# Kernel tuning notes

Measured on AMD Instinct MI355X. Metric: run time of the kernel, lower is better.

## Reference

```python
import jax, jax.numpy as jnp
import numpy as np

T, DM = 2048, 2048
H, KV, D = 16, 2, 128
E, I_MOE, I_SH = 16, 768, 768
TOP_K, N_GROUP, TOPK_GROUP = 4, 4, 2
ROPE_THETA = 1e6
EPS = 1e-5
ROUTED_SCALE = 1.0


def rmsnorm(x, w):
    v = jnp.mean(x * x, axis=-1, keepdims=True)
    return x * jax.lax.rsqrt(v + EPS) * w


def apply_rope(x, pos):
    # partial rotary: first D//2 dims rotated (neox style), rest passthrough
    rd = D // 2
    half = rd // 2
    inv = 1.0 / (ROPE_THETA ** (jnp.arange(0, rd, 2, dtype=jnp.float32) / rd))
    freqs = pos.astype(jnp.float32)[:, None] * inv  # [T, half]
    cos = jnp.cos(freqs)[:, None, :]
    sin = jnp.sin(freqs)[:, None, :]
    x1, x2 = x[..., :half], x[..., half:rd]
    rot = jnp.concatenate([x1 * cos - x2 * sin, x2 * cos + x1 * sin], axis=-1)
    return jnp.concatenate([rot, x[..., rd:]], axis=-1)


def mlp(x, wgu, wd):
    g, u = jnp.split(x @ wgu, 2, axis=-1)
    return (jax.nn.silu(g) * u) @ wd


def attention(x, pos, w_qkv, b_qkv, w_o, q_norm_w, k_norm_w):
    qkv = x @ w_qkv + b_qkv
    q, k, v = jnp.split(qkv, [H * D, H * D + KV * D], axis=-1)
    q = rmsnorm(q.reshape(T, H, D), q_norm_w)
    k = rmsnorm(k.reshape(T, KV, D), k_norm_w)
    v = v.reshape(T, KV, D)
    q = apply_rope(q, pos)
    k = apply_rope(k, pos)
    rep = H // KV
    k = jnp.repeat(k, rep, axis=1)
    v = jnp.repeat(v, rep, axis=1)
    scores = jnp.einsum('thd,shd->hts', q, k) * (D ** -0.5)
    causal = pos[:, None] >= pos[None, :]
    scores = jnp.where(causal[None], scores, jnp.finfo(scores.dtype).min)
    p = jax.nn.softmax(scores, axis=-1)
    o = jnp.einsum('hts,shd->thd', p, v).reshape(T, H * D)
    return o @ w_o


def moe(x, gate_w, gate_bias, shared_wgu, shared_wd, expert_wgu, expert_wd):
    # sigmoid grouped top-k routing with e_score_correction_bias (DeepSeek/GLM style)
    logits = x.astype(jnp.float32) @ gate_w
    scores = jax.nn.sigmoid(logits)
    sb = scores + gate_bias
    g = sb.reshape(T, N_GROUP, E // N_GROUP)
    group_scores = jnp.sum(jax.lax.top_k(g, 2)[0], axis=-1)  # [T, n_group]
    _, gi = jax.lax.top_k(group_scores, TOPK_GROUP)
    gmask = jnp.zeros((T, N_GROUP)).at[jnp.arange(T)[:, None], gi].set(1.0)
    emask = jnp.repeat(gmask, E // N_GROUP, axis=1)
    masked = jnp.where(emask > 0, sb, -jnp.inf)
    _, idx = jax.lax.top_k(masked, TOP_K)  # [T, top_k]
    w = jnp.take_along_axis(scores, idx, axis=1)
    w = w / jnp.sum(w, axis=1, keepdims=True)  # renormalize (norm_topk_prob)
    cw = jnp.zeros((T, E)).at[jnp.arange(T)[:, None], idx].add(w)  # dense combine weights
    gu = jnp.einsum('td,edi->tei', x, expert_wgu)  # [T, E, 2I]
    gt, ut = jnp.split(gu, 2, axis=-1)
    act = jax.nn.silu(gt) * ut * cw[:, :, None]
    routed = jnp.einsum('tei,eid->td', act, expert_wd)
    shared = mlp(x, shared_wgu, shared_wd)
    return routed * ROUTED_SCALE + shared


def setup_inputs() -> dict:
    key = jax.random.key(0)
    ks = jax.random.split(key, 12)
    s = 0.02
    return {
        'positions': jnp.arange(T, dtype=jnp.int32),
        'hidden_states': jax.random.normal(ks[0], (T, DM), jnp.float32),
        'residual': jax.random.normal(ks[1], (T, DM), jnp.float32),
        'ln1_w': jnp.ones((DM,), jnp.float32),
        'ln2_w': jnp.ones((DM,), jnp.float32),
        'w_qkv': jax.random.normal(ks[2], (DM, (H + 2 * KV) * D), jnp.float32) * s,
        'b_qkv': jnp.zeros(((H + 2 * KV) * D,), jnp.float32),
        'w_o': jax.random.normal(ks[3], (H * D, DM), jnp.float32) * s,
        'q_norm_w': jnp.ones((D,), jnp.float32),
        'k_norm_w': jnp.ones((D,), jnp.float32),
        'gate_w': jax.random.normal(ks[4], (DM, E), jnp.float32) * s,
        'gate_bias': jax.random.normal(ks[5], (E,), jnp.float32) * 0.1,
        'shared_wgu': jax.random.normal(ks[6], (DM, 2 * I_SH), jnp.float32) * s,
        'shared_wd': jax.random.normal(ks[7], (I_SH, DM), jnp.float32) * s,
        'expert_wgu': jax.random.normal(ks[8], (E, DM, 2 * I_MOE), jnp.float32) * s,
        'expert_wd': jax.random.normal(ks[9], (E, I_MOE, DM), jnp.float32) * s,
    }


def reference(positions, hidden_states, residual, ln1_w, ln2_w, w_qkv, b_qkv, w_o,
              q_norm_w, k_norm_w, gate_w, gate_bias, shared_wgu, shared_wd,
              expert_wgu, expert_wd):
    # fused add + RMSNorm (residual is not None path)
    residual = hidden_states + residual
    h = rmsnorm(residual, ln1_w)
    h = attention(h, positions, w_qkv, b_qkv, w_o, q_norm_w, k_norm_w)
    residual = h + residual
    h = rmsnorm(residual, ln2_w)
    h = moe(h, gate_w, gate_bias, shared_wgu, shared_wd, expert_wgu, expert_wd)
    return h, residual
```

## Files before the change

kernel.cpp:

```cpp
#include <hip/hip_runtime.h>
#include <stdint.h>
#include <math.h>

#define T_ 2048
#define DM 2048
#define NH 16
#define NKV 2
#define HD 128
#define QKVN 2560
#define NE 16
#define IM 768
#define ISH 768
#define MAXROWS 10240
#define ROWS_ALL 12288
#define NBLK 136
#define SM_SCALE 0.08838834764831845f

typedef __attribute__((ext_vector_type(8))) short short8;
typedef __attribute__((ext_vector_type(4))) float f32x4;

__device__ __forceinline__ float bf2f(unsigned short u){ return __uint_as_float(((unsigned int)u)<<16); }
__device__ __forceinline__ unsigned short f2bf(float f){
  unsigned int u = __float_as_uint(f);
  return (unsigned short)((u + 0x7FFFu + ((u>>16)&1u)) >> 16);
}
__device__ __forceinline__ void split2(float x, unsigned short& hi, unsigned short& lo){
  hi = f2bf(x);
  lo = f2bf(x - bf2f(hi));
}

__device__ __forceinline__ void gload16(const void* g, void* l){
  __builtin_amdgcn_global_load_lds((const __attribute__((address_space(1))) unsigned int*)g,
                                   (__attribute__((address_space(3))) unsigned int*)l, 16, 0, 0);
}

__device__ __forceinline__ int xcd_swz(int bid, int nwg){
  int q = nwg >> 3, r = nwg & 7, x = bid & 7, p = bid >> 3;
  return (x < r ? x*(q+1) : r*(q+1) + (x-r)*q) + p;
}

#define BAR()    asm volatile("s_barrier" ::: "memory")
#define VW(N)    asm volatile("s_waitcnt vmcnt(" #N ")" ::: "memory")
#define LW0()    do{ asm volatile("s_waitcnt lgkmcnt(0)" ::: "memory"); __builtin_amdgcn_sched_barrier(0); }while(0)

template<bool ILV>
__global__ void k_tconv(const float* __restrict__ src, unsigned short* __restrict__ dst,
                        const float* __restrict__ srcS, unsigned short* __restrict__ dstS,
                        int R, int C, size_t sS, size_t sD){
  int z = blockIdx.z;
  if (srcS && z == gridDim.z-1){ src = srcS; dst = dstS; }
  else { src += (size_t)z * sS; dst += (size_t)z * sD; }
  __shared__ float tile[64*65];
  int tid = threadIdx.x;
  int r0 = blockIdx.y*64, c0 = blockIdx.x*64;
  int lr = tid>>4, lc = (tid&15)*4;
  #pragma unroll
  for (int j=0;j<4;j++){
    int row = j*16 + lr;
    float4 v = *(const float4*)&src[(size_t)(r0+row)*C + c0 + lc];
    float* t = &tile[row*65 + lc];
    t[0]=v.x; t[1]=v.y; t[2]=v.z; t[3]=v.w;
  }
  __syncthreads();
  #pragma unroll
  for (int jj=0;jj<2;jj++){
    int slot = jj*256 + tid;
    int c = slot>>3, ro = (slot&7)*8;
    int cg = c0 + c;
    int cd = cg;
    if (ILV){ int b = cg>>3, inner = cg&7; cd = (b<96 ? b*16 : (b-96)*16+8) + inner; }
    short8 o;
    #pragma unroll
    for (int k=0;k<8;k++) o[k] = (short)f2bf(tile[(ro+k)*65 + c]);
    *(short8*)&dst[(size_t)cd*R + r0 + ro] = o;
  }
}

__global__ void k_tconv2(const float* __restrict__ srcA, unsigned short* __restrict__ dhiA,
                         unsigned short* __restrict__ dloA,
                         const float* __restrict__ srcB, unsigned short* __restrict__ dhiB,
                         unsigned short* __restrict__ dloB){
  const float* src; unsigned short* dhi; unsigned short* dlo; int R, C;
  if (blockIdx.z == 0){ src = srcA; dhi = dhiA; dlo = dloA; R = DM; C = QKVN; }
  else {
    if (blockIdx.x >= DM/64) return;
    src = srcB; dhi = dhiB; dlo = dloB; R = DM; C = DM;
  }
  __shared__ float tile[64*65];
  int tid = threadIdx.x;
  int r0 = blockIdx.y*64, c0 = blockIdx.x*64;
  int lr = tid>>4, lc = (tid&15)*4;
  #pragma unroll
  for (int j=0;j<4;j++){
    int row = j*16 + lr;
    float4 v = *(const float4*)&src[(size_t)(r0+row)*C + c0 + lc];
    float* t = &tile[row*65 + lc];
    t[0]=v.x; t[1]=v.y; t[2]=v.z; t[3]=v.w;
  }
  __syncthreads();
  #pragma unroll
  for (int jj=0;jj<2;jj++){
    int slot = jj*256 + tid;
    int c = slot>>3, ro = (slot&7)*8;
    short8 oh, ol;
    #pragma unroll
    for (int k=0;k<8;k++){
      unsigned short h_, l_;
      split2(tile[(ro+k)*65 + c], h_, l_);
      oh[k] = (short)h_; ol[k] = (short)l_;
    }
    size_t o = (size_t)(c0+c)*R + r0 + ro;
    *(short8*)&dhi[o] = oh;
    *(short8*)&dlo[o] = ol;
  }
}

template<bool ROUTE>
__global__ void k_add_rmsnorm(const float* __restrict__ a, const float* __restrict__ b,
                              const float* __restrict__ w, float* __restrict__ resout,
                              unsigned short* __restrict__ ohi, unsigned short* __restrict__ olo,
                              unsigned short* __restrict__ obf,
                              const float* __restrict__ gw, const float* __restrict__ gbias,
                              int* __restrict__ idx4, float* __restrict__ w4){
  int t = blockIdx.x, tid = threadIdx.x;
  const float4* a4 = (const float4*)(a + (size_t)t*DM);
  const float4* b4 = (const float4*)(b + (size_t)t*DM);
  float4 va = a4[tid], vb = b4[tid];
  float4 wa = a4[tid+256], wb = b4[tid+256];
  float4 v0, v1;
  v0.x=va.x+vb.x; v0.y=va.y+vb.y; v0.z=va.z+vb.z; v0.w=va.w+vb.w;
  v1.x=wa.x+wb.x; v1.y=wa.y+wb.y; v1.z=wa.z+wb.z; v1.w=wa.w+wb.w;
  float s = v0.x*v0.x+v0.y*v0.y+v0.z*v0.z+v0.w*v0.w
          + v1.x*v1.x+v1.y*v1.y+v1.z*v1.z+v1.w*v1.w;
  #pragma unroll
  for (int o=32;o;o>>=1) s += __shfl_xor(s,o);
  __shared__ float sm[4];
  if ((tid&63)==0) sm[tid>>6]=s;
  __syncthreads();
  s = sm[0]+sm[1]+sm[2]+sm[3];
  float rs = rsqrtf(s*(1.f/(float)DM) + 1e-5f);
  ((float4*)(resout + (size_t)t*DM))[tid] = v0;
  ((float4*)(resout + (size_t)t*DM))[tid+256] = v1;
  const float4* w4p_ = (const float4*)w;
  float4 w0 = w4p_[tid], w1 = w4p_[tid+256];
  float n[8] = { v0.x*rs*w0.x, v0.y*rs*w0.y, v0.z*rs*w0.z, v0.w*rs*w0.w,
                 v1.x*rs*w1.x, v1.y*rs*w1.y, v1.z*rs*w1.z, v1.w*rs*w1.w };
  if (ohi){
    ushort4 h0,h1,l0,l1;
    split2(n[0],h0.x,l0.x); split2(n[1],h0.y,l0.y); split2(n[2],h0.z,l0.z); split2(n[3],h0.w,l0.w);
    split2(n[4],h1.x,l1.x); split2(n[5],h1.y,l1.y); split2(n[6],h1.z,l1.z); split2(n[7],h1.w,l1.w);
    ((ushort4*)(ohi + (size_t)t*DM))[tid] = h0;
    ((ushort4*)(ohi + (size_t)t*DM))[tid+256] = h1;
    ((ushort4*)(olo + (size_t)t*DM))[tid] = l0;
    ((ushort4*)(olo + (size_t)t*DM))[tid+256] = l1;
  }
  if (obf){
    ushort4 o0 = make_ushort4(f2bf(n[0]),f2bf(n[1]),f2bf(n[2]),f2bf(n[3]));
    ushort4 o1 = make_ushort4(f2bf(n[4]),f2bf(n[5]),f2bf(n[6]),f2bf(n[7]));
    ((ushort4*)(obf + (size_t)t*DM))[tid] = o0;
    ((ushort4*)(obf + (size_t)t*DM))[tid+256] = o1;
  }
  if constexpr (ROUTE){
    __shared__ float xrow[DM];
    __shared__ float red[16][17];
    #pragma unroll
    for (int jj=0;jj<4;jj++) xrow[4*tid+jj] = n[jj];
    #pragma unroll
    for (int jj=0;jj<4;jj++) xrow[1024+4*tid+jj] = n[4+jj];
    __syncthreads();
    int e = tid & 15, grp = tid >> 4;
    float part = 0.f;
    #pragma unroll 8
    for (int c = grp; c < DM; c += 16)
      part += xrow[c] * gw[(size_t)c*16 + e];
    red[grp][e] = part;
    __syncthreads();
    if (tid==0){
      float sc[16], sb[16];
      for (int ee=0;ee<16;ee++){
        float lg = 0.f;
        for (int g2=0;g2<16;g2++) lg += red[g2][ee];
        sc[ee] = 1.f/(1.f+expf(-lg));
        sb[ee] = sc[ee] + gbias[ee];
      }
      float gs[4];
      for (int g=0;g<4;g++){
        float m1=-3.4e38f, m2=-3.4e38f;
        for (int j=0;j<4;j++){
          float v = sb[g*4+j];
          if (v>m1){ m2=m1; m1=v; } else if (v>m2) m2=v;
        }
        gs[g]=m1+m2;
      }
      int g1=0; for (int g=1;g<4;g++) if (gs[g]>gs[g1]) g1=g;
      int g2=-1; for (int g=0;g<4;g++){ if (g==g1) continue; if (g2<0 || gs[g]>gs[g2]) g2=g; }
      float msk[16];
      for (int ee=0;ee<16;ee++){ int g=ee>>2; msk[ee] = (g==g1||g==g2)? sb[ee] : -3.4e38f; }
      int id[4]; float wv[4]; float wsum=0.f;
      for (int s2=0;s2<4;s2++){
        int bb=0; float bv=-3.5e38f;
        for (int ee=0;ee<16;ee++) if (msk[ee]>bv){ bv=msk[ee]; bb=ee; }
        id[s2]=bb; wv[s2]=sc[bb]; wsum+=sc[bb]; msk[bb]=-3.5e38f;
      }
      float invs = 1.f/wsum;
      for (int s2=0;s2<4;s2++){
        idx4[t*4+s2]=id[s2];
        w4[t*4+s2]=wv[s2]*invs;
      }
    }
  }
}

template<bool GATHER, bool ACT>
__global__ __launch_bounds__(256) void k_gemm2(
    const unsigned short* __restrict__ A, const unsigned short* __restrict__ Be,
    const unsigned short* __restrict__ Bsh, unsigned short* __restrict__ C,
    int K, int lda, int ldb, int ldc,
    const int* __restrict__ offs, size_t sBe, const int* __restrict__ tok){
  int nx = gridDim.x;
  int nwg = nx * gridDim.y;
  int wid_ = xcd_swz(blockIdx.x + nx*blockIdx.y, nwg);
  int tN = wid_ % nx, tM = wid_ / nx;
  int rb = tM*128;
  if (rb >= offs[17]) return;
  const unsigned short* B;
  if (rb >= offs[16]) B = Bsh;
  else {
    int e=0;
    for (; e<15; ++e) if (offs[e+1] > rb) break;
    B = Be + (size_t)e*sBe;
  }
  __shared__ __align__(16) unsigned short As[2][4096];
  __shared__ __align__(16) unsigned short Bs[2][4096];
  int tid = threadIdx.x, lane = tid & 63, wwid = tid >> 6;
  int wr = wwid >> 1, wc = wwid & 1;
  const unsigned short* Bb = B + (size_t)tN*128*ldb;

  const unsigned short* Asrc0;
  const unsigned short* Asrc1;
  int r0s = tid>>2, r1s = r0s + 64;
  {
    if (GATHER){
      Asrc0 = A + (size_t)tok[rb + r0s]*lda;
      Asrc1 = A + (size_t)tok[rb + r1s]*lda;
    } else {
      Asrc0 = A + (size_t)(rb + r0s)*lda;
      Asrc1 = A + (size_t)(rb + r1s)*lda;
    }
  }
  int kc = tid&3;
  int sw = (r0s>>1)&3;
  int kcS = (kc ^ sw)*8;

  f32x4 acc[4][4];
  #pragma unroll
  for (int m=0;m<4;m++)
    #pragma unroll
    for (int n=0;n<4;n++) acc[m][n] = (f32x4){0.f,0.f,0.f,0.f};

  auto STAGE = [&](int b, int k0){
    gload16(Asrc0 + k0 + kcS, As[b] + (size_t)tid*8);
    gload16(Asrc1 + k0 + kcS, As[b] + (size_t)(256+tid)*8);
    gload16(Bb + (size_t)r0s*ldb + k0 + kcS, Bs[b] + (size_t)tid*8);
    gload16(Bb + (size_t)r1s*ldb + k0 + kcS, Bs[b] + (size_t)(256+tid)*8);
  };

  int nt = K >> 5, L = nt - 1;
  STAGE(0, 0);
  if (L >= 1) STAGE(1, 32);
  int i15 = lane & 15, g = lane >> 4;
  for (int i=0; i<nt; ++i){
    int cur = i & 1;
    if (i < L) { VW(4); } else { VW(0); }
    BAR();
    short8 af[4], bfr[4];
    #pragma unroll
    for (int m=0;m<4;m++){
      int row = wr*64 + m*16 + i15;
      int geff = g ^ ((row>>1)&3);
      af[m] = *(const short8*)(As[cur] + row*32 + geff*8);
    }
    #pragma unroll
    for (int n=0;n<4;n++){
      int row = wc*64 + n*16 + i15;
      int geff = g ^ ((row>>1)&3);
      bfr[n] = *(const short8*)(Bs[cur] + row*32 + geff*8);
    }
    LW0();
    BAR();
    if (i + 2 <= L) STAGE(cur, (i+2)*32);
    __builtin_amdgcn_s_setprio(1);
    #pragma unroll
    for (int m=0;m<4;m++)
      #pragma unroll
      for (int n=0;n<4;n++)
        acc[m][n] = __builtin_amdgcn_mfma_f32_16x16x32_bf16(af[m], bfr[n], acc[m][n], 0,0,0);
    __builtin_amdgcn_s_setprio(0);
  }

  if (ACT){
    int rbase = rb + wr*64, cb = tN*128 + wc*64;
    #pragma unroll
    for (int m=0;m<4;m++){
      int r0 = rbase + m*16 + ((lane>>4)<<2);
      #pragma unroll
      for (int n=0;n<4;n++){
        int f = ((cb + n*16)>>1) + (lane&7);
        #pragma unroll
        for (int r=0;r<4;r++){
          float v = acc[m][n][r];
          float vp = __shfl_xor(v, 8);
          if (!(lane&8)){
            float gg = v;
            float a = gg/(1.f+__expf(-gg))*vp;
            C[(size_t)(r0+r)*ldc + f] = f2bf(a);
          }
        }
      }
    }
  } else {
    int rbase = rb + wr*64, cb = tN*128 + wc*64;
    #pragma unroll
    for (int m=0;m<4;m++){
      int r0 = rbase + m*16 + ((lane>>4)<<2);
      #pragma unroll
      for (int n=0;n<4;n++){
        int c = cb + n*16 + (lane&15);
        #pragma unroll
        for (int r=0;r<4;r++) C[(size_t)(r0+r)*ldc + c] = f2bf(acc[m][n][r]);
      }
    }
  }
}

__global__ __launch_bounds__(256) void k_gemm_hp(
    const unsigned short* __restrict__ Ah, const unsigned short* __restrict__ Al,
    const unsigned short* __restrict__ Bh, const unsigned short* __restrict__ Bl,
    float* __restrict__ Cf,
    int K, int lda, int ldb, int ldc){
  int nx = gridDim.x, nwg = nx*gridDim.y;
  int w = xcd_swz(blockIdx.x + nx*blockIdx.y, nwg);
  int tN = w % nx, tM = w / nx;

  __shared__ __align__(16) unsigned short AsH[2][4096], AsL[2][4096];
  __shared__ __align__(16) unsigned short BsH[2][4096], BsL[2][4096];
  int tid = threadIdx.x, lane = tid & 63, wid = tid >> 6;
  int wr = wid >> 1, wc = wid & 1;
  const unsigned short* Abh = Ah + (size_t)tM*128*lda;
  const unsigned short* Abl = Al + (size_t)tM*128*lda;
  const unsigned short* Bbh = Bh + (size_t)tN*128*ldb;
  const unsigned short* Bbl = Bl + (size_t)tN*128*ldb;

  f32x4 acc[4][4];
  #pragma unroll
  for (int m=0;m<4;m++)
    #pragma unroll
    for (int n=0;n<4;n++) acc[m][n] = (f32x4){0.f,0.f,0.f,0.f};

  auto STAGE = [&](int b, int k0){
    #pragma unroll
    for (int j=0;j<2;j++){
      int cb = j*256 + tid;
      int row = cb>>2, kc = cb&3;
      int kcS = (kc ^ ((row>>1)&3))*8;
      size_t go = (size_t)row*lda + k0 + kcS;
      gload16(Abh + go, AsH[b] + (size_t)cb*8);
      gload16(Abl + go, AsL[b] + (size_t)cb*8);
      size_t bo = (size_t)row*ldb + k0 + kcS;
      gload16(Bbh + bo, BsH[b] + (size_t)cb*8);
      gload16(Bbl + bo, BsL[b] + (size_t)cb*8);
    }
  };

  int nt = K >> 5, L = nt - 1;
  STAGE(0, 0);
  if (L >= 1) STAGE(1, 32);
  int i15 = lane & 15, g = lane >> 4;
  for (int i=0; i<nt; ++i){
    int cur = i & 1;
    if (i < L) { VW(8); } else { VW(0); }
    BAR();
    short8 afh[4], afl[4], bfh[4], bfl[4];
    #pragma unroll
    for (int m=0;m<4;m++){
      int row = wr*64 + m*16 + i15;
      int ro = row*32 + (g ^ ((row>>1)&3))*8;
      afh[m] = *(const short8*)(AsH[cur] + ro);
      afl[m] = *(const short8*)(AsL[cur] + ro);
    }
    #pragma unroll
    for (int n=0;n<4;n++){
      int row = wc*64 + n*16 + i15;
      int ro = row*32 + (g ^ ((row>>1)&3))*8;
      bfh[n] = *(const short8*)(BsH[cur] + ro);
      bfl[n] = *(const short8*)(BsL[cur] + ro);
    }
    LW0();
    BAR();
    if (i + 2 <= L) STAGE(cur, (i+2)*32);
    __builtin_amdgcn_s_setprio(1);
    #pragma unroll
    for (int m=0;m<4;m++)
      #pragma unroll
      for (int n=0;n<4;n++){
        acc[m][n] = __builtin_amdgcn_mfma_f32_16x16x32_bf16(afh[m], bfh[n], acc[m][n], 0,0,0);
        acc[m][n] = __builtin_amdgcn_mfma_f32_16x16x32_bf16(afh[m], bfl[n], acc[m][n], 0,0,0);
        acc[m][n] = __builtin_amdgcn_mfma_f32_16x16x32_bf16(afl[m], bfh[n], acc[m][n], 0,0,0);
      }
    __builtin_amdgcn_s_setprio(0);
  }

  int rb = tM*128 + wr*64, cb = tN*128 + wc*64;
  #pragma unroll
  for (int m=0;m<4;m++){
    int r0 = rb + m*16 + ((lane>>4)<<2);
    #pragma unroll
    for (int n=0;n<4;n++){
      int c = cb + n*16 + (lane&15);
      #pragma unroll
      for (int r=0;r<4;r++) Cf[(size_t)(r0+r)*ldc + c] = acc[m][n][r];
    }
  }
}

__global__ __launch_bounds__(256) void k_qk_pers(
    const unsigned short* __restrict__ Qh, const unsigned short* __restrict__ Ql,
    const unsigned short* __restrict__ Kh, const unsigned short* __restrict__ Kl,
    float* __restrict__ Sp){
  int bb = blockIdx.x;
  int t0, ntile;
  if (bb < 128){ t0 = bb*9; ntile = 9; }
  else { t0 = 1152 + (bb-128)*8; ntile = 8; }
  const int ldq = NH*HD, ldk = NKV*HD;

  __shared__ __align__(16) unsigned short QsH[16384], QsL[16384];
  __shared__ __align__(16) unsigned short BsH[2][4096], BsL[2][4096];

  int tid = threadIdx.x, lane = tid & 63, wid = tid >> 6;
  int wr = wid >> 1, wc = wid & 1;
  int i15 = lane & 15, g = lane >> 4;

  f32x4 acc[4][4];
  #pragma unroll
  for (int m=0;m<4;m++)
    #pragma unroll
    for (int n=0;n<4;n++) acc[m][n] = (f32x4){0.f,0.f,0.f,0.f};

  int curZ = -1, curM = -1;
  const unsigned short* Kbh = Kh;
  const unsigned short* Kbl = Kl;
  int ti = 0;
  while (ti < ntile){
    int f = t0 + ti;
    int z = f / 136;
    int idx = f - z*136;
    int tM = 0;
    while ((tM+1)*(tM+2)/2 <= idx) tM++;
    int tri = tM*(tM+1)/2;
    int tnS = idx - tri;
    int run = ntile - ti;
    { int rem = tM+1 - tnS; if (rem < run) run = rem; }

    if (z != curZ || tM != curM){
      BAR();
      const unsigned short* Qbh = Qh + (size_t)(tM*128)*ldq + (size_t)z*HD;
      const unsigned short* Qbl = Ql + (size_t)(tM*128)*ldq + (size_t)z*HD;
      #pragma unroll
      for (int j=0;j<8;j++){
        int gi = j*256 + tid;
        int chunk = gi >> 9;
        int row = (gi >> 2) & 127;
        int gg = gi & 3;
        int col = chunk*32 + (gg ^ ((row>>1)&3))*8;
        gload16(Qbh + (size_t)row*ldq + col, QsH + (size_t)gi*8);
        gload16(Qbl + (size_t)row*ldq + col, QsL + (size_t)gi*8);
      }
      curZ = z; curM = tM;
      Kbh = Kh + (size_t)(z>>3)*HD;
      Kbl = Kl + (size_t)(z>>3)*HD;
    }

    auto BSTAGE = [&](int b, int ci){
      int tn = tnS + (ci >> 2), c = ci & 3;
      const unsigned short* sh = Kbh + (size_t)(tn*128)*ldk;
      const unsigned short* sl = Kbl + (size_t)(tn*128)*ldk;
      #pragma unroll
      for (int j=0;j<2;j++){
        int gi = j*256 + tid;
        int row = gi >> 2, gg = gi & 3;
        int col = c*32 + (gg ^ ((row>>1)&3))*8;
        gload16(sh + (size_t)row*ldk + col, BsH[b] + (size_t)gi*8);
        gload16(sl + (size_t)row*ldk + col, BsL[b] + (size_t)gi*8);
      }
    };

    int NC = run*4;
    BSTAGE(0, 0);
    BSTAGE(1, 1);
    for (int ci=0; ci<NC; ++ci){
      int cur = ci & 1, c = ci & 3, tn = tnS + (ci >> 2);
      if (ci < NC-1) { VW(4); } else { VW(0); }
      BAR();
      short8 afh[4], afl[4], bfh[4], bfl[4];
      #pragma unroll
      for (int m=0;m<4;m++){
        int row = wr*64 + m*16 + i15;
        int ro = c*4096 + row*32 + (g ^ ((row>>1)&3))*8;
        afh[m] = *(const short8*)(QsH + ro);
        afl[m] = *(const short8*)(QsL + ro);
      }
      #pragma unroll
      for (int n=0;n<4;n++){
        int row = wc*64 + n*16 + i15;
        int ro = row*32 + (g ^ ((row>>1)&3))*8;
        bfh[n] = *(const short8*)(BsH[cur] + ro);
        bfl[n] = *(const short8*)(BsL[cur] + ro);
      }
      LW0();
      BAR();
      if (ci + 2 < NC) BSTAGE(cur, ci+2);
      __builtin_amdgcn_s_setprio(1);
      #pragma unroll
      for (int m=0;m<4;m++)
        #pragma unroll
        for (int n=0;n<4;n++){
          acc[m][n] = __builtin_amdgcn_mfma_f32_16x16x32_bf16(afh[m], bfh[n], acc[m][n], 0,0,0);
          acc[m][n] = __builtin_amdgcn_mfma_f32_16x16x32_bf16(afh[m], bfl[n], acc[m][n], 0,0,0);
          acc[m][n] = __builtin_amdgcn_mfma_f32_16x16x32_bf16(afl[m], bfh[n], acc[m][n], 0,0,0);
        }
      __builtin_amdgcn_s_setprio(0);
      if (c == 3){
        float* Cb = Sp + ((size_t)z*NBLK + tri + tn)*16384;
        #pragma unroll
        for (int m=0;m<4;m++){
          int r0 = wr*64 + m*16 + (g<<2);
          #pragma unroll
          for (int n=0;n<4;n++){
            int ccol = wc*64 + n*16 + i15;
            #pragma unroll
            for (int r=0;r<4;r++) Cb[(size_t)(r0+r)*128 + ccol] = acc[m][n][r];
          }
        }
        #pragma unroll
        for (int m=0;m<4;m++)
          #pragma unroll
          for (int n=0;n<4;n++) acc[m][n] = (f32x4){0.f,0.f,0.f,0.f};
      }
    }
    ti += run;
  }
}

__global__ __launch_bounds__(256) void k_pv_hp(
    const float* __restrict__ Sp,
    const unsigned short* __restrict__ Vh, const unsigned short* __restrict__ Vl,
    float* __restrict__ part, float* __restrict__ rsums){
  int c = blockIdx.x, tM = blockIdx.y, z = blockIdx.z;
  int kbeg = c*512;
  int kend = min((tM+1)*128, (c+1)*512);
  if (kbeg >= kend) return;
  int tMk = tM*128;
  size_t tri = (size_t)tM*(tM+1)/2;
  const float* Ab = Sp + ((size_t)z*NBLK + tri)*16384;
  const unsigned short* Bbh = Vh + (size_t)(z>>3)*HD*T_;
  const unsigned short* Bbl = Vl + (size_t)(z>>3)*HD*T_;

  __shared__ __align__(16) float Asf[2][4096];
  __shared__ __align__(16) unsigned short BsH[2][4096], BsL[2][4096];
  int tid = threadIdx.x, lane = tid & 63, wid = tid >> 6;
  int wr = wid >> 1, wc = wid & 1;
  int i15 = lane & 15, g2 = (lane>>4)*2;

  int r0s = tid>>2, r1s = r0s + 64;
  int kcB = ((tid&3) ^ ((r0s>>1)&3))*8;
  int rowA = tid>>3, gA = tid&7;

  f32x4 acc[4][4];
  #pragma unroll
  for (int m=0;m<4;m++)
    #pragma unroll
    for (int n=0;n<4;n++) acc[m][n] = (f32x4){0.f,0.f,0.f,0.f};
  float rsum[4] = {0.f,0.f,0.f,0.f};

  auto STAGE = [&](int b, int k0){
    #pragma unroll
    for (int j=0;j<4;j++){
      int r = j*32 + rowA;
      int gS = gA ^ (r & 7);
      size_t ga = (size_t)(k0>>7)*16384 + (size_t)r*128 + (k0&127) + gS*4;
      gload16(Ab + ga, Asf[b] + ((size_t)j*256 + tid)*4);
    }
    size_t bo0 = (size_t)r0s*T_ + k0 + kcB;
    size_t bo1 = (size_t)r1s*T_ + k0 + kcB;
    gload16(Bbh + bo0, BsH[b] + (size_t)tid*8);
    gload16(Bbh + bo1, BsH[b] + (size_t)(256+tid)*8);
    gload16(Bbl + bo0, BsL[b] + (size_t)tid*8);
    gload16(Bbl + bo1, BsL[b] + (size_t)(256+tid)*8);
  };

  int nt = (kend - kbeg) >> 5, L = nt - 1;
  STAGE(0, kbeg);
  if (L >= 1) STAGE(1, kbeg + 32);
  for (int i=0; i<nt; ++i){
    int cur = i & 1;
    int k0 = kbeg + i*32;
    if (i < L) { VW(8); } else { VW(0); }
    BAR();
    int diag = (k0 >= tMk);
    short8 afh[4], afl[4], bfh[4], bfl[4];
    #pragma unroll
    for (int m=0;m<4;m++){
      int r = wr*64 + m*16 + i15;
      int s0 = r*8 + ((g2  ) ^ (r&7));
      int s1 = r*8 + ((g2+1) ^ (r&7));
      f32x4 a0 = *(const f32x4*)(Asf[cur] + s0*4);
      f32x4 a1 = *(const f32x4*)(Asf[cur] + s1*4);
      float pv[8] = {a0[0],a0[1],a0[2],a0[3],a1[0],a1[1],a1[2],a1[3]};
      if (diag){
        int kb = k0 & 127;
        #pragma unroll
        for (int j=0;j<8;j++){
          int kl = kb + ((j<4) ? g2*4 + j : (g2+1)*4 + (j-4));
          if (kl > r) pv[j] = -3.0e38f;
        }
      }
      short8 h8, l8;
      #pragma unroll
      for (int j=0;j<8;j++){
        float p = __expf(pv[j]*SM_SCALE);
        rsum[m] += p;
        unsigned short hh, ll; split2(p, hh, ll);
        h8[j] = (short)hh; l8[j] = (short)ll;
      }
      afh[m] = h8; afl[m] = l8;
    }
    #pragma unroll
    for (int n=0;n<4;n++){
      int row = wc*64 + n*16 + i15;
      int ro = row*32 + ((lane>>4) ^ ((row>>1)&3))*8;
      bfh[n] = *(const short8*)(BsH[cur] + ro);
      bfl[n] = *(const short8*)(BsL[cur] + ro);
    }
    LW0();
    BAR();
    if (i + 2 <= L) STAGE(cur, kbeg + (i+2)*32);
    __builtin_amdgcn_s_setprio(1);
    #pragma unroll
    for (int m=0;m<4;m++)
      #pragma unroll
      for (int n=0;n<4;n++){
        acc[m][n] = __builtin_amdgcn_mfma_f32_16x16x32_bf16(afh[m], bfh[n], acc[m][n], 0,0,0);
        acc[m][n] = __builtin_amdgcn_mfma_f32_16x16x32_bf16(afh[m], bfl[n], acc[m][n], 0,0,0);
        acc[m][n] = __builtin_amdgcn_mfma_f32_16x16x32_bf16(afl[m], bfh[n], acc[m][n], 0,0,0);
      }
    __builtin_amdgcn_s_setprio(0);
  }

  #pragma unroll
  for (int m=0;m<4;m++){
    float v = rsum[m];
    v += __shfl_xor(v, 16);
    v += __shfl_xor(v, 32);
    if ((lane>>4)==0 && wc==0)
      rsums[((size_t)c*NH + z)*T_ + tMk + wr*64 + m*16 + i15] = v;
  }

  float* Cb = part + (size_t)c*T_*DM + (size_t)tMk*DM + (size_t)z*HD;
  #pragma unroll
  for (int m=0;m<4;m++){
    int r0 = wr*64 + m*16 + ((lane>>4)<<2);
    #pragma unroll
    for (int n=0;n<4;n++){
      int ccol = wc*64 + n*16 + (lane&15);
      #pragma unroll
      for (int r=0;r<4;r++) Cb[(size_t)(r0+r)*DM + ccol] = acc[m][n][r];
    }
  }
}

__global__ void k_pv_reduce(const float* __restrict__ part, const float* __restrict__ rsums,
                            unsigned short* __restrict__ aoh, unsigned short* __restrict__ aol){
  int t = blockIdx.x, tid = threadIdx.x;
  int nc = ((t>>7) + 4) >> 2;
  #pragma unroll
  for (int half=0; half<2; ++half){
    int idx = tid + half*256;
    int z = idx >> 5;
    float tot = 0.f;
    for (int c=0; c<nc; ++c) tot += rsums[((size_t)c*NH + z)*T_ + t];
    float inv = 1.f / tot;
    float4 s = ((const float4*)(part + (size_t)t*DM))[idx];
    for (int c=1; c<nc; ++c){
      float4 v = ((const float4*)(part + (size_t)c*T_*DM + (size_t)t*DM))[idx];
      s.x+=v.x; s.y+=v.y; s.z+=v.z; s.w+=v.w;
    }
    s.x*=inv; s.y*=inv; s.z*=inv; s.w*=inv;
    ushort4 h_, l_;
    split2(s.x,h_.x,l_.x); split2(s.y,h_.y,l_.y); split2(s.z,h_.z,l_.z); split2(s.w,h_.w,l_.w);
    ((ushort4*)(aoh + (size_t)t*DM))[idx] = h_;
    ((ushort4*)(aol + (size_t)t*DM))[idx] = l_;
  }
}

__global__ void k_qkv_post_hp(const float* __restrict__ qkv, const float* __restrict__ bias,
                              const float* __restrict__ qnw, const float* __restrict__ knw,
                              const int* __restrict__ pos_,
                              unsigned short* __restrict__ qhi, unsigned short* __restrict__ qlo,
                              unsigned short* __restrict__ khi, unsigned short* __restrict__ klo,
                              unsigned short* __restrict__ vThi, unsigned short* __restrict__ vTlo){
  int t = blockIdx.x;
  int half = threadIdx.x >> 7;
  int d = threadIdx.x & 127;
  int wseg = (threadIdx.x >> 6) & 1;
  float posf = (float)pos_[t];
  __shared__ float buf[2][128];
  __shared__ float ssum[2][2];
  __shared__ float inv_sh[32];
  if (threadIdx.x < 32)
    inv_sh[threadIdx.x] = (float)pow(1000000.0, -(double)threadIdx.x/32.0);
  __syncthreads();
  for (int it=0; it<10; ++it){
    int seg = it*2 + half;
    float x = qkv[(size_t)t*QKVN + seg*128 + d] + bias[seg*128 + d];
    float p = x*x;
    #pragma unroll
    for (int o=32;o;o>>=1) p += __shfl_xor(p,o);
    if ((threadIdx.x&63)==0) ssum[half][wseg] = p;
    __syncthreads();
    float rs = rsqrtf((ssum[half][0]+ssum[half][1])*(1.f/128.f) + 1e-5f);
    float w = (seg<16) ? qnw[d] : ((seg<18) ? knw[d] : 1.f);
    float nv = x*rs*w;
    buf[half][d] = nv;
    __syncthreads();
    float outv = (seg<18) ? nv : x;
    if (seg < 18 && d < 64){
      int i = d & 31;
      float ang = posf * inv_sh[i];
      float sn, cs; sincosf(ang, &sn, &cs);
      if (d < 32) outv = nv*cs - buf[half][d+32]*sn;
      else        outv = nv*cs + buf[half][d-32]*sn;
    }
    unsigned short h_, l_; split2(outv, h_, l_);
    if (seg < 16){ size_t o = ((size_t)t*NH + seg)*HD + d; qhi[o]=h_; qlo[o]=l_; }
    else if (seg < 18){ size_t o = ((size_t)t*NKV + (seg-16))*HD + d; khi[o]=h_; klo[o]=l_; }
    else { size_t o = ((size_t)(seg-18)*HD + d)*T_ + t; vThi[o]=h_; vTlo[o]=l_; }
    __syncthreads();
  }
}

__global__ void k_offplace(const int* __restrict__ idx4, int* __restrict__ offs,
                           int* __restrict__ rrow, int* __restrict__ tok){
  __shared__ int hist[16];
  __shared__ int hoff[16];
  __shared__ int fill[16];
  int tid = threadIdx.x;
  if (tid < 16) hist[tid] = 0;
  __syncthreads();
  for (int i = tid; i < ROWS_ALL; i += 256) tok[i] = 0;
  for (int i = tid; i < T_*4; i += 256)
    atomicAdd(&hist[idx4[i]], 1);
  __syncthreads();
  if (tid == 0){
    int o = 0;
    for (int e=0;e<16;e++){ hoff[e]=o; offs[e]=o; o += ((hist[e]+127)>>7)<<7; }
    offs[16]=o;
    offs[17]=o + T_;
  }
  if (tid < 16) fill[tid] = 0;
  __syncthreads();
  int off16 = offs[16];
  for (int t = tid; t < T_; t += 256){
    #pragma unroll
    for (int s=0;s<4;s++){
      int e = idx4[t*4+s];
      int p = atomicAdd(&fill[e],1);
      int r = hoff[e]+p;
      rrow[t*4+s]=r;
      tok[r]=t;
    }
    tok[off16+t] = t;
  }
}

__global__ void k_combine(const unsigned short* __restrict__ eout,
                          const int* __restrict__ rrow, const float* __restrict__ w4,
                          const int* __restrict__ offs, float* __restrict__ outh){
  int t = blockIdx.x;
  int rs = offs[16] + t;
  int r0=rrow[t*4+0], r1=rrow[t*4+1], r2=rrow[t*4+2], r3=rrow[t*4+3];
  float w0=w4[t*4+0], w1=w4[t*4+1], w2=w4[t*4+2], w3=w4[t*4+3];
  for (int d=threadIdx.x; d<DM; d+=256){
    float v = bf2f(eout[(size_t)rs*DM+d])
            + w0*bf2f(eout[(size_t)r0*DM+d]) + w1*bf2f(eout[(size_t)r1*DM+d])
            + w2*bf2f(eout[(size_t)r2*DM+d]) + w3*bf2f(eout[(size_t)r3*DM+d]);
    outh[(size_t)t*DM+d] = v;
  }
}

extern "C" void kernel_launch(void* const* d_in, const int* in_sizes, int n_in,
                              void* d_out, int out_size, void* d_ws, size_t ws_size,
                              hipStream_t stream){
  const int*   positions = (const int*)d_in[0];
  const float* hidden    = (const float*)d_in[1];
  const float* residual  = (const float*)d_in[2];
  const float* ln1       = (const float*)d_in[3];
  const float* ln2       = (const float*)d_in[4];
  const float* w_qkv     = (const float*)d_in[5];
  const float* b_qkv     = (const float*)d_in[6];
  const float* w_o       = (const float*)d_in[7];
  const float* qnw       = (const float*)d_in[8];
  const float* knw       = (const float*)d_in[9];
  const float* gate_w    = (const float*)d_in[10];
  const float* gate_b    = (const float*)d_in[11];
  const float* sh_wgu    = (const float*)d_in[12];
  const float* sh_wd     = (const float*)d_in[13];
  const float* e_wgu     = (const float*)d_in[14];
  const float* e_wd      = (const float*)d_in[15];
  float* out_h   = (float*)d_out;
  float* out_res = (float*)d_out + (size_t)T_*DM;

  char* ws = (char*)d_ws;
  size_t off = 0;
  auto alloc = [&](size_t b){ size_t r = off; off += (b + 255) & ~(size_t)255; return r; };

  size_t o_h2b  = alloc((size_t)T_*DM*2);
  size_t o_idx  = alloc((size_t)T_*4*4);
  size_t o_w4   = alloc((size_t)T_*4*4);
  size_t o_offs = alloc(72);
  size_t o_rrow = alloc((size_t)T_*4*4);
  size_t o_tok  = alloc((size_t)ROWS_ALL*4);

  size_t U0 = off;
  size_t a = U0;
  auto allocA = [&](size_t b){ size_t r = a; a += (b + 255) & ~(size_t)255; return r; };
  size_t o_h1h  = allocA((size_t)T_*DM*2);
  size_t o_h1l  = allocA((size_t)T_*DM*2);
  size_t o_wqh  = allocA((size_t)QKVN*DM*2);
  size_t o_wql  = allocA((size_t)QKVN*DM*2);
  size_t o_qkvf = allocA((size_t)T_*QKVN*4);
  size_t o_qh   = allocA((size_t)T_*NH*HD*2);
  size_t o_ql   = allocA((size_t)T_*NH*HD*2);
  size_t o_kh   = allocA((size_t)T_*NKV*HD*2);
  size_t o_kl   = allocA((size_t)T_*NKV*HD*2);
  size_t o_vth  = allocA((size_t)NKV*HD*T_*2);
  size_t o_vtl  = allocA((size_t)NKV*HD*T_*2);
  size_t o_woh  = allocA((size_t)DM*DM*2);
  size_t o_wol  = allocA((size_t)DM*DM*2);
  size_t o_aoh  = allocA((size_t)T_*DM*2);
  size_t o_aol  = allocA((size_t)T_*DM*2);
  size_t o_attnP= allocA((size_t)T_*DM*4);
  size_t o_rsum = allocA((size_t)4*NH*T_*4);
  size_t o_Sp   = allocA((size_t)NH*NBLK*16384*4);
  size_t o_pvp  = allocA((size_t)4*T_*DM*4);
  size_t b_ = U0;
  auto allocB = [&](size_t b){ size_t r = b_; b_ += (b + 255) & ~(size_t)255; return r; };
  size_t o_ewgu = allocB((size_t)NE*2*IM*DM*2);
  size_t o_ewd  = allocB((size_t)NE*DM*IM*2);
  size_t o_shgu = allocB((size_t)2*ISH*DM*2);
  size_t o_shwd = allocB((size_t)DM*ISH*2);
  size_t o_actx = allocB((size_t)ROWS_ALL*IM*2);
  size_t o_eout = allocB((size_t)ROWS_ALL*DM*2);

  unsigned short* h2b   = (unsigned short*)(ws+o_h2b);
  int*   idx4  = (int*)(ws+o_idx);
  float* w4p   = (float*)(ws+o_w4);
  int*   offs  = (int*)(ws+o_offs);
  int*   rrow  = (int*)(ws+o_rrow);
  int*   tok   = (int*)(ws+o_tok);
  unsigned short* h1h = (unsigned short*)(ws+o_h1h);
  unsigned short* h1l = (unsigned short*)(ws+o_h1l);
  unsigned short* wqh = (unsigned short*)(ws+o_wqh);
  unsigned short* wql = (unsigned short*)(ws+o_wql);
  float*          qkvf= (float*)(ws+o_qkvf);
  unsigned short* qh  = (unsigned short*)(ws+o_qh);
  unsigned short* ql  = (unsigned short*)(ws+o_ql);
  unsigned short* kh  = (unsigned short*)(ws+o_kh);
  unsigned short* kl  = (unsigned short*)(ws+o_kl);
  unsigned short* vth = (unsigned short*)(ws+o_vth);
  unsigned short* vtl = (unsigned short*)(ws+o_vtl);
  unsigned short* woh = (unsigned short*)(ws+o_woh);
  unsigned short* wol = (unsigned short*)(ws+o_wol);
  unsigned short* aoh = (unsigned short*)(ws+o_aoh);
  unsigned short* aol = (unsigned short*)(ws+o_aol);
  float*          attnP=(float*)(ws+o_attnP);
  float*          rsums=(float*)(ws+o_rsum);
  float*          Sp  = (float*)(ws+o_Sp);
  float*          pvpart = (float*)(ws+o_pvp);
  unsigned short* ewguT=(unsigned short*)(ws+o_ewgu);
  unsigned short* ewdT = (unsigned short*)(ws+o_ewd);
  unsigned short* shguT=(unsigned short*)(ws+o_shgu);
  unsigned short* shwdT=(unsigned short*)(ws+o_shwd);
  unsigned short* actx= (unsigned short*)(ws+o_actx);
  unsigned short* eout= (unsigned short*)(ws+o_eout);

  k_tconv2<<<dim3(QKVN/64, DM/64, 2),256,0,stream>>>(w_qkv, wqh, wql, w_o, woh, wol);

  k_add_rmsnorm<false><<<T_,256,0,stream>>>(hidden, residual, ln1, out_res, h1h, h1l, nullptr,
                                            nullptr, nullptr, nullptr, nullptr);

  k_gemm_hp<<<dim3(QKVN/128,T_/128,1),256,0,stream>>>(
      h1h, h1l, wqh, wql, qkvf, DM, DM, DM, QKVN);
  k_qkv_post_hp<<<T_,256,0,stream>>>(qkvf, b_qkv, qnw, knw, positions, qh, ql, kh, kl, vth, vtl);

  k_qk_pers<<<dim3(256),256,0,stream>>>(qh, ql, kh, kl, Sp);
  k_pv_hp<<<dim3(4,T_/128,NH),256,0,stream>>>(Sp, vth, vtl, pvpart, rsums);
  k_pv_reduce<<<T_,256,0,stream>>>(pvpart, rsums, aoh, aol);
  k_gemm_hp<<<dim3(DM/128,T_/128,1),256,0,stream>>>(
      aoh, aol, woh, wol, attnP, DM, DM, DM, DM);

  k_add_rmsnorm<true><<<T_,256,0,stream>>>(attnP, out_res, ln2, out_res, nullptr, nullptr, h2b,
                                           gate_w, gate_b, idx4, w4p);

  k_offplace<<<1,256,0,stream>>>(idx4, offs, rrow, tok);

  k_tconv<true ><<<dim3(2*IM/64, DM/64, NE+1),256,0,stream>>>(
      e_wgu, ewguT, sh_wgu, shguT, DM, 2*IM, (size_t)DM*2*IM, (size_t)2*IM*DM);
  k_tconv<false><<<dim3(DM/64, IM/64, NE+1),256,0,stream>>>(
      e_wd,  ewdT,  sh_wd,  shwdT, IM, DM,   (size_t)IM*DM,   (size_t)DM*IM);

  k_gemm2<true, true ><<<dim3(2*IM/128, ROWS_ALL/128, 1),256,0,stream>>>(
      h2b, ewguT, shguT, actx, DM, DM, DM, IM, offs, (size_t)2*IM*DM, tok);
  k_gemm2<false, false><<<dim3(DM/128, ROWS_ALL/128, 1),256,0,stream>>>(
      actx, ewdT, shwdT, eout, IM, IM, IM, DM, offs, (size_t)DM*IM, nullptr);

  k_combine<<<T_,256,0,stream>>>(eout, rrow, w4p, offs, out_h);
}
```

Measured before the change: 664.4 us.

## Merge weight conversions and routing offsets into one kernel; balance PV split

Folds the two MoE weight transpose/convert kernels and the single-block offset/placement kernel into one launch, with the offset work done by a spare block. This removes two launches and hides the serial one-block kernel behind the conversion work. Separately, the PV kernel now splits the causal key range evenly into 128-wide tiles across a number of chunks that depends on the row tile, instead of fixed 512-wide chunks, to balance work. The trade-off is a larger grid with idle blocks, and the offset work now runs inside one block of a busy kernel.

```diff
diff --git a/kernel.cpp b/kernel.cpp
--- a/kernel.cpp
+++ b/kernel.cpp
@@ -43,16 +43,66 @@
 #define VW(N)    asm volatile("s_waitcnt vmcnt(" #N ")" ::: "memory")
 #define LW0()    do{ asm volatile("s_waitcnt lgkmcnt(0)" ::: "memory"); __builtin_amdgcn_sched_barrier(0); }while(0)
 
-template<bool ILV>
-__global__ void k_tconv(const float* __restrict__ src, unsigned short* __restrict__ dst,
-                        const float* __restrict__ srcS, unsigned short* __restrict__ dstS,
-                        int R, int C, size_t sS, size_t sD){
-  int z = blockIdx.z;
-  if (srcS && z == gridDim.z-1){ src = srcS; dst = dstS; }
-  else { src += (size_t)z * sS; dst += (size_t)z * sD; }
+__device__ void do_offplace(const int* __restrict__ idx4, int* __restrict__ offs,
+                            int* __restrict__ rrow, int* __restrict__ tok){
+  __shared__ int hist[16];
+  __shared__ int hoff[16];
+  __shared__ int fill[16];
+  int tid = threadIdx.x;
+  if (tid < 16) hist[tid] = 0;
+  __syncthreads();
+  for (int i = tid; i < ROWS_ALL; i += 256) tok[i] = 0;
+  for (int i = tid; i < T_*4; i += 256)
+    atomicAdd(&hist[idx4[i]], 1);
+  __syncthreads();
+  if (tid == 0){
+    int o = 0;
+    for (int e=0;e<16;e++){ hoff[e]=o; offs[e]=o; o += ((hist[e]+127)>>7)<<7; }
+    offs[16]=o;
+    offs[17]=o + T_;
+  }
+  if (tid < 16) fill[tid] = 0;
+  __syncthreads();
+  int off16 = offs[16];
+  for (int t = tid; t < T_; t += 256){
+    #pragma unroll
+    for (int s=0;s<4;s++){
+      int e = idx4[t*4+s];
+      int p = atomicAdd(&fill[e],1);
+      int r = hoff[e]+p;
+      rrow[t*4+s]=r;
+      tok[r]=t;
+    }
+    tok[off16+t] = t;
+  }
+}
+
+__global__ void k_wconv(const float* __restrict__ e_wgu, unsigned short* __restrict__ ewguT,
+                        const float* __restrict__ sh_wgu, unsigned short* __restrict__ shguT,
+                        const float* __restrict__ e_wd, unsigned short* __restrict__ ewdT,
+                        const float* __restrict__ sh_wd, unsigned short* __restrict__ shwdT,
+                        const int* __restrict__ idx4, int* __restrict__ offs,
+                        int* __restrict__ rrow, int* __restrict__ tok){
   __shared__ float tile[64*65];
+  int z = blockIdx.z, x = blockIdx.x, y = blockIdx.y;
   int tid = threadIdx.x;
-  int r0 = blockIdx.y*64, c0 = blockIdx.x*64;
+  const float* src; unsigned short* dst;
+  int R, C, r0, c0;
+  bool ilv;
+  if (x < 24){
+    src = (z==16)? sh_wgu : e_wgu + (size_t)z*((size_t)DM*2*IM);
+    dst = (z==16)? shguT : ewguT + (size_t)z*((size_t)2*IM*DM);
+    R = DM; C = 2*IM; r0 = y*64; c0 = x*64; ilv = true;
+  } else {
+    int flat = (x-24) + 24*y;
+    if (flat >= 384){
+      if (z==16 && x==47 && y==31) do_offplace(idx4, offs, rrow, tok);
+      return;
+    }
+    src = (z==16)? sh_wd : e_wd + (size_t)z*((size_t)IM*DM);
+    dst = (z==16)? shwdT : ewdT + (size_t)z*((size_t)DM*IM);
+    R = IM; C = DM; r0 = (flat/32)*64; c0 = (flat%32)*64; ilv = false;
+  }
   int lr = tid>>4, lc = (tid&15)*4;
   #pragma unroll
   for (int j=0;j<4;j++){
@@ -68,7 +118,7 @@
     int c = slot>>3, ro = (slot&7)*8;
     int cg = c0 + c;
     int cd = cg;
-    if (ILV){ int b = cg>>3, inner = cg&7; cd = (b<96 ? b*16 : (b-96)*16+8) + inner; }
+    if (ilv){ int b = cg>>3, inner = cg&7; cd = (b<96 ? b*16 : (b-96)*16+8) + inner; }
     short8 o;
     #pragma unroll
     for (int k=0;k<8;k++) o[k] = (short)f2bf(tile[(ro+k)*65 + c]);
@@ -556,9 +606,14 @@
     const unsigned short* __restrict__ Vh, const unsigned short* __restrict__ Vl,
     float* __restrict__ part, float* __restrict__ rsums){
   int c = blockIdx.x, tM = blockIdx.y, z = blockIdx.z;
-  int kbeg = c*512;
-  int kend = min((tM+1)*128, (c+1)*512);
-  if (kbeg >= kend) return;
+  int nc = (tM+4)>>2;
+  if (c >= nc) return;
+  int ntile = tM+1;
+  int base = ntile/nc, rem = ntile - base*nc;
+  int start = c*base + (c<rem ? c : rem);
+  int len = base + (c<rem ? 1 : 0);
+  int kbeg = start*128;
+  int kend = kbeg + len*128;
   int tMk = tM*128;
   size_t tri = (size_t)tM*(tM+1)/2;
   const float* Ab = Sp + ((size_t)z*NBLK + tri)*16384;
@@ -745,40 +800,6 @@
     else if (seg < 18){ size_t o = ((size_t)t*NKV + (seg-16))*HD + d; khi[o]=h_; klo[o]=l_; }
     else { size_t o = ((size_t)(seg-18)*HD + d)*T_ + t; vThi[o]=h_; vTlo[o]=l_; }
     __syncthreads();
-  }
-}
-
-__global__ void k_offplace(const int* __restrict__ idx4, int* __restrict__ offs,
-                           int* __restrict__ rrow, int* __restrict__ tok){
-  __shared__ int hist[16];
-  __shared__ int hoff[16];
-  __shared__ int fill[16];
-  int tid = threadIdx.x;
-  if (tid < 16) hist[tid] = 0;
-  __syncthreads();
-  for (int i = tid; i < ROWS_ALL; i += 256) tok[i] = 0;
-  for (int i = tid; i < T_*4; i += 256)
-    atomicAdd(&hist[idx4[i]], 1);
-  __syncthreads();
-  if (tid == 0){
-    int o = 0;
-    for (int e=0;e<16;e++){ hoff[e]=o; offs[e]=o; o += ((hist[e]+127)>>7)<<7; }
-    offs[16]=o;
-    offs[17]=o + T_;
-  }
-  if (tid < 16) fill[tid] = 0;
-  __syncthreads();
-  int off16 = offs[16];
-  for (int t = tid; t < T_; t += 256){
-    #pragma unroll
-    for (int s=0;s<4;s++){
-      int e = idx4[t*4+s];
-      int p = atomicAdd(&fill[e],1);
-      int r = hoff[e]+p;
-      rrow[t*4+s]=r;
-      tok[r]=t;
-    }
-    tok[off16+t] = t;
   }
 }
 
@@ -911,12 +932,8 @@
   k_add_rmsnorm<true><<<T_,256,0,stream>>>(attnP, out_res, ln2, out_res, nullptr, nullptr, h2b,
                                            gate_w, gate_b, idx4, w4p);
 
-  k_offplace<<<1,256,0,stream>>>(idx4, offs, rrow, tok);
-
-  k_tconv<true ><<<dim3(2*IM/64, DM/64, NE+1),256,0,stream>>>(
-      e_wgu, ewguT, sh_wgu, shguT, DM, 2*IM, (size_t)DM*2*IM, (size_t)2*IM*DM);
-  k_tconv<false><<<dim3(DM/64, IM/64, NE+1),256,0,stream>>>(
-      e_wd,  ewdT,  sh_wd,  shwdT, IM, DM,   (size_t)IM*DM,   (size_t)DM*IM);
+  k_wconv<<<dim3(48,32,NE+1),256,0,stream>>>(
+      e_wgu, ewguT, sh_wgu, shguT, e_wd, ewdT, sh_wd, shwdT, idx4, offs, rrow, tok);
 
   k_gemm2<true, true ><<<dim3(2*IM/128, ROWS_ALL/128, 1),256,0,stream>>>(
       h2b, ewguT, shguT, actx, DM, DM, DM, IM, offs, (size_t)2*IM*DM, tok);
```

Measured after the change: 663.1 us. No clear change (-0.2%).
